# Optimization experiments

Measured on AMD Instinct MI355X. Metric: run time of the kernel, lower is better.

The kernel has to match this reference:

```python
import jax, jax.numpy as jnp
import numpy as np

N, E, B = 50000, 800000, 64
IN_C, HID, HEADS = 128, 64, 4
NEG_SLOPE = 0.2


def _gat_layer(x, src, dst, W, a_src, a_dst, bias, heads, out_c, concat):
    # x: [N, F_in] -> h: [N, heads, out_c]
    h = (x @ W).reshape(-1, heads, out_c)
    alpha_src = jnp.sum(h * a_src[None], axis=-1)  # [N, heads]
    alpha_dst = jnp.sum(h * a_dst[None], axis=-1)  # [N, heads]
    e = jax.nn.leaky_relu(alpha_src[src] + alpha_dst[dst], NEG_SLOPE)  # [Etot, heads]
    # segment softmax over incoming edges of each destination node
    m = jax.lax.stop_gradient(jax.ops.segment_max(e, dst, num_segments=N))
    m = jnp.where(jnp.isfinite(m), m, 0.0)
    ex = jnp.exp(e - m[dst])
    denom = jax.ops.segment_sum(ex, dst, num_segments=N)
    alpha = ex / jnp.maximum(denom[dst], 1e-16)
    msg = h[src] * alpha[:, :, None]  # [Etot, heads, out_c]
    out = jax.ops.segment_sum(msg, dst, num_segments=N)  # [N, heads, out_c]
    if concat:
        return out.reshape(-1, heads * out_c) + bias
    return out.mean(axis=1) + bias


def setup_inputs() -> dict:
    key = jax.random.key(0)
    ks = jax.random.split(key, 16)
    g = lambda k, shp, fan: jax.random.normal(k, shp, jnp.float32) * (1.0 / np.sqrt(fan))
    return {
        "x": jax.random.normal(ks[0], (N, IN_C), jnp.float32),
        "edge_index": jax.random.randint(ks[1], (2, E), 0, N, jnp.int64),
        "batch": jnp.sort(jax.random.randint(ks[2], (N,), 0, B, jnp.int64)),
        "W1": g(ks[3], (IN_C, HEADS * HID), IN_C),
        "as1": g(ks[4], (HEADS, HID), HID),
        "ad1": g(ks[5], (HEADS, HID), HID),
        "b1": jnp.zeros((HEADS * HID,), jnp.float32),
        "W2": g(ks[6], (HEADS * HID, HEADS * HID), HEADS * HID),
        "as2": g(ks[7], (HEADS, HID), HID),
        "ad2": g(ks[8], (HEADS, HID), HID),
        "b2": jnp.zeros((HID,), jnp.float32),
        "Wm1": g(ks[9], (HID, HID), HID),
        "bm1": jnp.zeros((HID,), jnp.float32),
        "Wm2": g(ks[10], (HID, 1), HID),
        "bm2": jnp.zeros((1,), jnp.float32),
    }


def reference(x, edge_index, batch, W1, as1, ad1, b1, W2, as2, ad2, b2, Wm1, bm1, Wm2, bm2):
    # add self loops (PyG GATConv default)
    loops = jnp.arange(N, dtype=edge_index.dtype)
    src = jnp.concatenate([edge_index[0], loops])
    dst = jnp.concatenate([edge_index[1], loops])
    h = _gat_layer(x, src, dst, W1, as1, ad1, b1, HEADS, HID, concat=True)
    h = jax.nn.relu(h)
    h = _gat_layer(h, src, dst, W2, as2, ad2, b2, HEADS, HID, concat=False)
    # global mean pool over graphs
    counts = jax.ops.segment_sum(jnp.ones((N,), h.dtype), batch, num_segments=B)
    pooled = jax.ops.segment_sum(h, batch, num_segments=B) / jnp.maximum(counts, 1.0)[:, None]
    # graph MLP
    out = jax.nn.relu(pooled @ Wm1 + bm1) @ Wm2 + bm2  # [B, 1]
    return out
```

## Files before the change

kernel.cpp:

```cpp
#include <hip/hip_runtime.h>
#include <hip/hip_bf16.h>

#define N_NODES 50000
#define N_EDGES 800000
#define ETOT    (N_EDGES + N_NODES)
#define NB      64
#define IN_C    128
#define HID     64
#define HEADS   4
#define F1      (HEADS * HID)
#define NEG     0.2f
#define SCAN_NBLK ((N_NODES + 255) / 256)

typedef __attribute__((ext_vector_type(8))) short  short8v;
typedef __attribute__((ext_vector_type(4))) float  float4v;

__device__ __forceinline__ float lrelu(float x) { return x >= 0.f ? x : NEG * x; }

__device__ __forceinline__ unsigned short f2bf(float f) {
    unsigned u = __float_as_uint(f);
    u += 0x7FFFu + ((u >> 16) & 1u);
    return (unsigned short)(u >> 16);
}
__device__ __forceinline__ float bf2f(unsigned short h) {
    return __uint_as_float(((unsigned)h) << 16);
}

__global__ void deg_kernel(const int* __restrict__ ei, int* __restrict__ deg) {
    int e = blockIdx.x * 256 + threadIdx.x;
    if (e >= ETOT) return;
    int d = (e < N_EDGES) ? ei[N_EDGES + e] : (e - N_EDGES);
    atomicAdd(&deg[d], 1);
}

__global__ void scan1_kernel(const int* __restrict__ deg, int* __restrict__ part) {
    __shared__ int sh[256];
    int t = threadIdx.x;
    int i = blockIdx.x * 256 + t;
    sh[t] = (i < N_NODES) ? deg[i] : 0;
    __syncthreads();
    #pragma unroll
    for (int o = 128; o; o >>= 1) {
        if (t < o) sh[t] += sh[t + o];
        __syncthreads();
    }
    if (t == 0) part[blockIdx.x] = sh[0];
}

__global__ void scan2_kernel(int* __restrict__ part, int* __restrict__ off) {
    __shared__ int sh[256];
    int t = threadIdx.x;
    int v = (t < SCAN_NBLK) ? part[t] : 0;
    sh[t] = v;
    __syncthreads();
    #pragma unroll
    for (int o = 1; o < 256; o <<= 1) {
        int u = (t >= o) ? sh[t - o] : 0;
        __syncthreads();
        sh[t] += u;
        __syncthreads();
    }
    if (t < SCAN_NBLK) part[t] = sh[t] - v;
    if (t == 255) off[N_NODES] = sh[255];
}

__global__ void scan3_kernel(int* __restrict__ deg, const int* __restrict__ part,
                             int* __restrict__ off) {
    __shared__ int sh[256];
    int t = threadIdx.x;
    int i = blockIdx.x * 256 + t;
    int v = (i < N_NODES) ? deg[i] : 0;
    sh[t] = v;
    __syncthreads();
    #pragma unroll
    for (int o = 1; o < 256; o <<= 1) {
        int u = (t >= o) ? sh[t - o] : 0;
        __syncthreads();
        sh[t] += u;
        __syncthreads();
    }
    if (i < N_NODES) {
        off[i] = part[blockIdx.x] + sh[t] - v;
        deg[i] = 0;
    }
}

__global__ void scatter_kernel(const int* __restrict__ ei, const int* __restrict__ off,
                               int* __restrict__ cursor, int* __restrict__ esrc) {
    int e = blockIdx.x * 256 + threadIdx.x;
    if (e >= ETOT) return;
    int s, d;
    if (e < N_EDGES) { s = ei[e]; d = ei[N_EDGES + e]; }
    else             { s = d = e - N_EDGES; }
    int pos = off[d] + atomicAdd(&cursor[d], 1);
    esrc[pos] = s;
}

__global__ void convw2_kernel(const float* __restrict__ W1,
                              unsigned short* __restrict__ W1h, unsigned short* __restrict__ W1l,
                              const float* __restrict__ W2,
                              unsigned short* __restrict__ W2h, unsigned short* __restrict__ W2l) {
    int i = blockIdx.x * 256 + threadIdx.x;
    const int N1 = IN_C * 256;
    if (i < N1) {
        int k = i >> 8, n = i & 255;
        float v = W1[i];
        unsigned short h = f2bf(v);
        W1h[n * IN_C + k] = h;
        W1l[n * IN_C + k] = f2bf(v - bf2f(h));
    } else {
        int j = i - N1;
        if (j >= F1 * 256) return;
        int k = j >> 8, n = j & 255;
        float v = W2[j];
        unsigned short h = f2bf(v);
        W2h[n * F1 + k] = h;
        W2l[n * F1 + k] = f2bf(v - bf2f(h));
    }
}

template <bool SPLIT_A>
__global__ __launch_bounds__(256) void gemm_mfma(const float* __restrict__ Af32,
                                                 const unsigned short* __restrict__ Abg,
                                                 const unsigned short* __restrict__ Wth,
                                                 const unsigned short* __restrict__ Wtl,
                                                 const float* __restrict__ a_s,
                                                 const float* __restrict__ a_d,
                                                 unsigned short* __restrict__ Cb,
                                                 float* __restrict__ asrcO,
                                                 float* __restrict__ adstO,
                                                 int M, int K) {
    __shared__ unsigned short Ab[64][40];
    __shared__ unsigned short Bh[256][40], Bl[256][40];
    int t  = threadIdx.x;
    int m0 = blockIdx.x * 64;
    int w  = t >> 6, l = t & 63;
    int lr = l & 15, lk = (l >> 4) * 8;

    float asv[4], adv[4];
    #pragma unroll
    for (int nf = 0; nf < 4; ++nf) {
        asv[nf] = a_s[w * 64 + nf * 16 + lr];
        adv[nf] = a_d[w * 64 + nf * 16 + lr];
    }

    float4v acc[4][4];
    #pragma unroll
    for (int mf = 0; mf < 4; ++mf)
        #pragma unroll
        for (int nf = 0; nf < 4; ++nf)
            acc[mf][nf] = (float4v){0.f, 0.f, 0.f, 0.f};

    for (int k0 = 0; k0 < K; k0 += 32) {
        if (SPLIT_A) {
            #pragma unroll
            for (int p = 0; p < 2; ++p) {
                int idx = t + p * 256;
                int r = idx >> 3, c4 = (idx & 7) * 4;
                int gr = m0 + r;
                float4 v = make_float4(0.f, 0.f, 0.f, 0.f);
                if (gr < M) v = *(const float4*)&Af32[(size_t)gr * K + k0 + c4];
                ushort4 hi;
                hi.x = f2bf(v.x); hi.y = f2bf(v.y); hi.z = f2bf(v.z); hi.w = f2bf(v.w);
                *(ushort4*)&Ab[r][c4] = hi;
            }
        } else {
            int r = t >> 2, c8 = (t & 3) * 8;
            int gr = m0 + r;
            short8v vh = {0,0,0,0,0,0,0,0};
            if (gr < M) vh = *(const short8v*)&Abg[(size_t)gr * K + k0 + c8];
            *(short8v*)&Ab[r][c8] = vh;
        }
        #pragma unroll
        for (int p = 0; p < 4; ++p) {
            int idx = t + p * 256;
            int r = idx >> 2, c8 = (idx & 3) * 8;
            short8v vh = *(const short8v*)&Wth[(size_t)r * K + k0 + c8];
            short8v vl = *(const short8v*)&Wtl[(size_t)r * K + k0 + c8];
            *(short8v*)&Bh[r][c8] = vh;
            *(short8v*)&Bl[r][c8] = vl;
        }
        __syncthreads();

        short8v a_f[4], b_hf[4], b_lf[4];
        #pragma unroll
        for (int mf = 0; mf < 4; ++mf)
            a_f[mf] = *(short8v*)&Ab[mf * 16 + lr][lk];
        #pragma unroll
        for (int nf = 0; nf < 4; ++nf) {
            b_hf[nf] = *(short8v*)&Bh[w * 64 + nf * 16 + lr][lk];
            b_lf[nf] = *(short8v*)&Bl[w * 64 + nf * 16 + lr][lk];
        }
        #pragma unroll
        for (int mf = 0; mf < 4; ++mf)
            #pragma unroll
            for (int nf = 0; nf < 4; ++nf) {
                acc[mf][nf] = __builtin_amdgcn_mfma_f32_16x16x32_bf16(a_f[mf], b_hf[nf], acc[mf][nf], 0, 0, 0);
                acc[mf][nf] = __builtin_amdgcn_mfma_f32_16x16x32_bf16(a_f[mf], b_lf[nf], acc[mf][nf], 0, 0, 0);
            }
        __syncthreads();
    }

    #pragma unroll
    for (int mf = 0; mf < 4; ++mf)
        #pragma unroll
        for (int r = 0; r < 4; ++r) {
            float ps = acc[mf][0][r] * asv[0] + acc[mf][1][r] * asv[1]
                     + acc[mf][2][r] * asv[2] + acc[mf][3][r] * asv[3];
            float pd = acc[mf][0][r] * adv[0] + acc[mf][1][r] * adv[1]
                     + acc[mf][2][r] * adv[2] + acc[mf][3][r] * adv[3];
            #pragma unroll
            for (int o = 8; o; o >>= 1) {
                ps += __shfl_xor(ps, o);
                pd += __shfl_xor(pd, o);
            }
            int gr = m0 + mf * 16 + (l >> 4) * 4 + r;
            if (lr == 0 && gr < M) {
                asrcO[gr * 4 + w] = ps;
                adstO[gr * 4 + w] = pd;
            }
        }

    #pragma unroll
    for (int mf = 0; mf < 4; ++mf)
        #pragma unroll
        for (int nf = 0; nf < 4; ++nf)
            #pragma unroll
            for (int r = 0; r < 4; ++r) {
                int gr = m0 + mf * 16 + (l >> 4) * 4 + r;
                if (gr < M) Cb[(size_t)gr * F1 + w * 64 + nf * 16 + lr] = f2bf(acc[mf][nf][r]);
            }
}

template <int LAYER>
__global__ void agg_kernel(const unsigned short* __restrict__ hb,
                           const float* __restrict__ asrc,
                           const float* __restrict__ adst,
                           const int* __restrict__ off,
                           const int* __restrict__ esrc,
                           const float* __restrict__ bias,
                           float* __restrict__ outF,
                           unsigned short* __restrict__ oh) {
    __shared__ int   soff[64];
    __shared__ float cf[64][4];
    int d    = blockIdx.x;
    int lane = threadIdx.x;
    int w    = lane >> 4;
    int e0 = off[d], e1 = off[d + 1];
    float4 ad = *(const float4*)(adst + (size_t)d * 4);
    float den = 0.f;
    float a0 = 0.f, a1 = 0.f, a2 = 0.f, a3 = 0.f;
    const char* hbase = (const char*)hb;
    int lb = lane * 8;

    for (int base = e0; base < e1; base += 64) {
        int cnt = min(64, e1 - base);
        if (lane < cnt) {
            int s = esrc[base + lane];
            soff[lane] = s * (F1 * 2);
            float4 as = *(const float4*)(asrc + (size_t)s * 4);
            cf[lane][0] = __expf(lrelu(as.x + ad.x));
            cf[lane][1] = __expf(lrelu(as.y + ad.y));
            cf[lane][2] = __expf(lrelu(as.z + ad.z));
            cf[lane][3] = __expf(lrelu(as.w + ad.w));
        }
        __syncthreads();
        int i = 0;
        for (; i + 4 <= cnt; i += 4) {
            int o0 = soff[i], o1 = soff[i + 1], o2 = soff[i + 2], o3 = soff[i + 3];
            ushort4 h0 = *(const ushort4*)(hbase + o0 + lb);
            ushort4 h1 = *(const ushort4*)(hbase + o1 + lb);
            ushort4 h2 = *(const ushort4*)(hbase + o2 + lb);
            ushort4 h3 = *(const ushort4*)(hbase + o3 + lb);
            float c0 = cf[i][w], c1 = cf[i + 1][w], c2 = cf[i + 2][w], c3 = cf[i + 3][w];
            den += (c0 + c1) + (c2 + c3);
            a0 += c0 * bf2f(h0.x) + c1 * bf2f(h1.x) + c2 * bf2f(h2.x) + c3 * bf2f(h3.x);
            a1 += c0 * bf2f(h0.y) + c1 * bf2f(h1.y) + c2 * bf2f(h2.y) + c3 * bf2f(h3.y);
            a2 += c0 * bf2f(h0.z) + c1 * bf2f(h1.z) + c2 * bf2f(h2.z) + c3 * bf2f(h3.z);
            a3 += c0 * bf2f(h0.w) + c1 * bf2f(h1.w) + c2 * bf2f(h2.w) + c3 * bf2f(h3.w);
        }
        for (; i < cnt; ++i) {
            int o = soff[i];
            float c = cf[i][w];
            ushort4 hv = *(const ushort4*)(hbase + o + lb);
            den += c;
            a0 += c * bf2f(hv.x);
            a1 += c * bf2f(hv.y);
            a2 += c * bf2f(hv.z);
            a3 += c * bf2f(hv.w);
        }
        __syncthreads();
    }

    float r = 1.f / fmaxf(den, 1e-16f);
    if (LAYER == 1) {
        ushort4 hi;
        hi.x = f2bf(fmaxf(a0 * r + bias[lane * 4 + 0], 0.f));
        hi.y = f2bf(fmaxf(a1 * r + bias[lane * 4 + 1], 0.f));
        hi.z = f2bf(fmaxf(a2 * r + bias[lane * 4 + 2], 0.f));
        hi.w = f2bf(fmaxf(a3 * r + bias[lane * 4 + 3], 0.f));
        *(ushort4*)&oh[(size_t)d * F1 + lane * 4] = hi;
    } else {
        float v0 = a0 * r, v1 = a1 * r, v2 = a2 * r, v3 = a3 * r;
        v0 += __shfl_xor(v0, 16); v0 += __shfl_xor(v0, 32);
        v1 += __shfl_xor(v1, 16); v1 += __shfl_xor(v1, 32);
        v2 += __shfl_xor(v2, 16); v2 += __shfl_xor(v2, 32);
        v3 += __shfl_xor(v3, 16); v3 += __shfl_xor(v3, 32);
        if (lane < 16) {
            float4 o;
            o.x = 0.25f * v0 + bias[lane * 4 + 0];
            o.y = 0.25f * v1 + bias[lane * 4 + 1];
            o.z = 0.25f * v2 + bias[lane * 4 + 2];
            o.w = 0.25f * v3 + bias[lane * 4 + 3];
            *(float4*)&outF[(size_t)d * HID + lane * 4] = o;
        }
    }
}

__device__ __forceinline__ int lowerb(const int* __restrict__ a, int n, int v) {
    int lo = 0, hi = n;
    while (lo < hi) { int m = (lo + hi) >> 1; if (a[m] < v) lo = m + 1; else hi = m; }
    return lo;
}

__global__ void poolmlp_kernel(const float* __restrict__ h2,
                               const int* __restrict__ batch,
                               const float* __restrict__ Wm1, const float* __restrict__ bm1,
                               const float* __restrict__ Wm2, const float* __restrict__ bm2,
                               float* __restrict__ out) {
    __shared__ float sh[4][HID];
    int b = blockIdx.x;
    int t = threadIdx.x, w = t >> 6, c = t & 63;
    int lo = lowerb(batch, N_NODES, b);
    int hi = lowerb(batch, N_NODES, b + 1);
    float s = 0.f;
    for (int n = lo + w; n < hi; n += 4) s += h2[(size_t)n * HID + c];
    sh[w][c] = s;
    __syncthreads();
    if (w == 0) {
        float inv = 1.f / fmaxf((float)(hi - lo), 1.f);
        float P = (sh[0][c] + sh[1][c] + sh[2][c] + sh[3][c]) * inv;
        sh[0][c] = P;
        float s1 = bm1[c];
        #pragma unroll
        for (int k = 0; k < HID; ++k) s1 += sh[0][k] * Wm1[k * HID + c];
        float r = fmaxf(s1, 0.f) * Wm2[c];
        #pragma unroll
        for (int o = 32; o; o >>= 1) r += __shfl_xor(r, o);
        if (c == 0) out[b] = r + bm2[0];
    }
}

extern "C" void kernel_launch(void* const* d_in, const int* in_sizes, int n_in,
                              void* d_out, int out_size, void* d_ws, size_t ws_size,
                              hipStream_t stream) {
    const float* x   = (const float*)d_in[0];
    const int*   ei  = (const int*)d_in[1];
    const int*   bat = (const int*)d_in[2];
    const float* W1  = (const float*)d_in[3];
    const float* as1 = (const float*)d_in[4];
    const float* ad1 = (const float*)d_in[5];
    const float* b1  = (const float*)d_in[6];
    const float* W2  = (const float*)d_in[7];
    const float* as2 = (const float*)d_in[8];
    const float* ad2 = (const float*)d_in[9];
    const float* b2  = (const float*)d_in[10];
    const float* Wm1 = (const float*)d_in[11];
    const float* bm1 = (const float*)d_in[12];
    const float* Wm2 = (const float*)d_in[13];
    const float* bm2 = (const float*)d_in[14];
    float* out = (float*)d_out;

    char* ws = (char*)d_ws;
    size_t cursor = 0;
    auto alloc = [&](size_t bytes) {
        void* p = ws + cursor;
        cursor += (bytes + 511) & ~(size_t)511;
        return p;
    };
    int*   deg    = (int*)alloc((size_t)N_NODES * 4);
    int*   off    = (int*)alloc((size_t)(N_NODES + 1) * 4);
    int*   part   = (int*)alloc((size_t)SCAN_NBLK * 4);
    int*   esrc   = (int*)alloc((size_t)ETOT * 4);
    unsigned short* bufHb = (unsigned short*)alloc((size_t)N_NODES * F1 * 2);
    char*  U      = (char*)alloc((size_t)N_NODES * F1 * 4);
    unsigned short* oh = (unsigned short*)U;
    float* bufO   = (float*)U;
    float* asrc   = (float*)alloc((size_t)N_NODES * HEADS * 4);
    float* adst   = (float*)alloc((size_t)N_NODES * HEADS * 4);
    unsigned short* W1th = (unsigned short*)alloc((size_t)256 * IN_C * 2);
    unsigned short* W1tl = (unsigned short*)alloc((size_t)256 * IN_C * 2);
    unsigned short* W2th = (unsigned short*)alloc((size_t)256 * F1 * 2);
    unsigned short* W2tl = (unsigned short*)alloc((size_t)256 * F1 * 2);

    hipMemsetAsync(deg, 0, (size_t)N_NODES * 4, stream);

    deg_kernel<<<(ETOT + 255) / 256, 256, 0, stream>>>(ei, deg);
    scan1_kernel<<<SCAN_NBLK, 256, 0, stream>>>(deg, part);
    scan2_kernel<<<1, 256, 0, stream>>>(part, off);
    scan3_kernel<<<SCAN_NBLK, 256, 0, stream>>>(deg, part, off);
    scatter_kernel<<<(ETOT + 255) / 256, 256, 0, stream>>>(ei, off, deg, esrc);

    convw2_kernel<<<((IN_C + F1) * 256 + 255) / 256, 256, 0, stream>>>(
        W1, W1th, W1tl, W2, W2th, W2tl);

    const int GB = (N_NODES + 63) / 64;
    gemm_mfma<true><<<GB, 256, 0, stream>>>(x, nullptr, W1th, W1tl,
                                            as1, ad1, bufHb, asrc, adst, N_NODES, IN_C);
    agg_kernel<1><<<N_NODES, 64, 0, stream>>>(bufHb, asrc, adst, off, esrc, b1,
                                              nullptr, oh);

    gemm_mfma<false><<<GB, 256, 0, stream>>>(nullptr, oh, W2th, W2tl,
                                             as2, ad2, bufHb, asrc, adst, N_NODES, F1);
    agg_kernel<2><<<N_NODES, 64, 0, stream>>>(bufHb, asrc, adst, off, esrc, b2,
                                              bufO, nullptr);

    poolmlp_kernel<<<NB, 256, 0, stream>>>(bufO, bat, Wm1, bm1, Wm2, bm2, out);
}
```

Before: 343.3 us.

## Fuse CSR build and weight conversion into one cooperative kernel with grid syncs

Replaces the memset, degree count, three scan kernels, scatter and weight-conversion launches with a single cooperative kernel of 1024 blocks, separating the phases with grid-wide syncs. The aim is to cut the launch and drain overhead of several small dependent kernels. In exchange the work runs at a fixed grid size, each grid.sync adds its own cost, and the launch fails if 1024 blocks cannot be co-resident.

New measurement: 856.2 us. 149% more time.

```diff
diff --git a/kernel.cpp b/kernel.cpp
--- a/kernel.cpp
+++ b/kernel.cpp
@@ -1,5 +1,8 @@
 #include <hip/hip_runtime.h>
 #include <hip/hip_bf16.h>
+#include <hip/hip_cooperative_groups.h>
+
+namespace cg = cooperative_groups;
 
 #define N_NODES 50000
 #define N_EDGES 800000
@@ -11,6 +14,7 @@
 #define F1      (HEADS * HID)
 #define NEG     0.2f
 #define SCAN_NBLK ((N_NODES + 255) / 256)
+#define PREP_BLOCKS 1024
 
 typedef __attribute__((ext_vector_type(8))) short  short8v;
 typedef __attribute__((ext_vector_type(4))) float  float4v;
@@ -26,96 +30,100 @@
     return __uint_as_float(((unsigned)h) << 16);
 }
 
-__global__ void deg_kernel(const int* __restrict__ ei, int* __restrict__ deg) {
-    int e = blockIdx.x * 256 + threadIdx.x;
-    if (e >= ETOT) return;
-    int d = (e < N_EDGES) ? ei[N_EDGES + e] : (e - N_EDGES);
-    atomicAdd(&deg[d], 1);
-}
-
-__global__ void scan1_kernel(const int* __restrict__ deg, int* __restrict__ part) {
+__global__ void prep_kernel(const int* __restrict__ ei,
+                            const float* __restrict__ W1, const float* __restrict__ W2,
+                            int* __restrict__ deg, int* __restrict__ off,
+                            int* __restrict__ part, int* __restrict__ esrc,
+                            unsigned short* __restrict__ W1h, unsigned short* __restrict__ W1l,
+                            unsigned short* __restrict__ W2h, unsigned short* __restrict__ W2l) {
+    cg::grid_group grid = cg::this_grid();
     __shared__ int sh[256];
-    int t = threadIdx.x;
-    int i = blockIdx.x * 256 + t;
-    sh[t] = (i < N_NODES) ? deg[i] : 0;
-    __syncthreads();
-    #pragma unroll
-    for (int o = 128; o; o >>= 1) {
-        if (t < o) sh[t] += sh[t + o];
-        __syncthreads();
-    }
-    if (t == 0) part[blockIdx.x] = sh[0];
-}
-
-__global__ void scan2_kernel(int* __restrict__ part, int* __restrict__ off) {
-    __shared__ int sh[256];
-    int t = threadIdx.x;
-    int v = (t < SCAN_NBLK) ? part[t] : 0;
-    sh[t] = v;
-    __syncthreads();
-    #pragma unroll
-    for (int o = 1; o < 256; o <<= 1) {
-        int u = (t >= o) ? sh[t - o] : 0;
-        __syncthreads();
-        sh[t] += u;
-        __syncthreads();
-    }
-    if (t < SCAN_NBLK) part[t] = sh[t] - v;
-    if (t == 255) off[N_NODES] = sh[255];
-}
-
-__global__ void scan3_kernel(int* __restrict__ deg, const int* __restrict__ part,
-                             int* __restrict__ off) {
-    __shared__ int sh[256];
-    int t = threadIdx.x;
-    int i = blockIdx.x * 256 + t;
-    int v = (i < N_NODES) ? deg[i] : 0;
-    sh[t] = v;
-    __syncthreads();
-    #pragma unroll
-    for (int o = 1; o < 256; o <<= 1) {
-        int u = (t >= o) ? sh[t - o] : 0;
-        __syncthreads();
-        sh[t] += u;
-        __syncthreads();
-    }
-    if (i < N_NODES) {
-        off[i] = part[blockIdx.x] + sh[t] - v;
-        deg[i] = 0;
-    }
-}
-
-__global__ void scatter_kernel(const int* __restrict__ ei, const int* __restrict__ off,
-                               int* __restrict__ cursor, int* __restrict__ esrc) {
-    int e = blockIdx.x * 256 + threadIdx.x;
-    if (e >= ETOT) return;
-    int s, d;
-    if (e < N_EDGES) { s = ei[e]; d = ei[N_EDGES + e]; }
-    else             { s = d = e - N_EDGES; }
-    int pos = off[d] + atomicAdd(&cursor[d], 1);
-    esrc[pos] = s;
-}
-
-__global__ void convw2_kernel(const float* __restrict__ W1,
-                              unsigned short* __restrict__ W1h, unsigned short* __restrict__ W1l,
-                              const float* __restrict__ W2,
-                              unsigned short* __restrict__ W2h, unsigned short* __restrict__ W2l) {
-    int i = blockIdx.x * 256 + threadIdx.x;
-    const int N1 = IN_C * 256;
-    if (i < N1) {
-        int k = i >> 8, n = i & 255;
-        float v = W1[i];
-        unsigned short h = f2bf(v);
-        W1h[n * IN_C + k] = h;
-        W1l[n * IN_C + k] = f2bf(v - bf2f(h));
-    } else {
-        int j = i - N1;
-        if (j >= F1 * 256) return;
-        int k = j >> 8, n = j & 255;
-        float v = W2[j];
-        unsigned short h = f2bf(v);
-        W2h[n * F1 + k] = h;
-        W2l[n * F1 + k] = f2bf(v - bf2f(h));
+    int t   = threadIdx.x;
+    int tid = blockIdx.x * 256 + t;
+    const int NT = PREP_BLOCKS * 256;
+
+    for (int i = tid; i < N_NODES; i += NT) deg[i] = 0;
+    {
+        const int N1 = IN_C * 256;
+        for (int i = tid; i < N1 + F1 * 256; i += NT) {
+            if (i < N1) {
+                int k = i >> 8, n = i & 255;
+                float v = W1[i];
+                unsigned short h = f2bf(v);
+                W1h[n * IN_C + k] = h;
+                W1l[n * IN_C + k] = f2bf(v - bf2f(h));
+            } else {
+                int j = i - N1;
+                int k = j >> 8, n = j & 255;
+                float v = W2[j];
+                unsigned short h = f2bf(v);
+                W2h[n * F1 + k] = h;
+                W2l[n * F1 + k] = f2bf(v - bf2f(h));
+            }
+        }
+    }
+    grid.sync();
+
+    for (int e = tid; e < ETOT; e += NT) {
+        int d = (e < N_EDGES) ? ei[N_EDGES + e] : (e - N_EDGES);
+        atomicAdd(&deg[d], 1);
+    }
+    grid.sync();
+
+    if (blockIdx.x < SCAN_NBLK) {
+        int i = blockIdx.x * 256 + t;
+        sh[t] = (i < N_NODES) ? deg[i] : 0;
+        __syncthreads();
+        #pragma unroll
+        for (int o = 128; o; o >>= 1) {
+            if (t < o) sh[t] += sh[t + o];
+            __syncthreads();
+        }
+        if (t == 0) part[blockIdx.x] = sh[0];
+    }
+    grid.sync();
+
+    if (blockIdx.x == 0) {
+        int v = (t < SCAN_NBLK) ? part[t] : 0;
+        sh[t] = v;
+        __syncthreads();
+        #pragma unroll
+        for (int o = 1; o < 256; o <<= 1) {
+            int u = (t >= o) ? sh[t - o] : 0;
+            __syncthreads();
+            sh[t] += u;
+            __syncthreads();
+        }
+        if (t < SCAN_NBLK) part[t] = sh[t] - v;
+        if (t == 255) off[N_NODES] = sh[255];
+    }
+    grid.sync();
+
+    if (blockIdx.x < SCAN_NBLK) {
+        int i = blockIdx.x * 256 + t;
+        int v = (i < N_NODES) ? deg[i] : 0;
+        sh[t] = v;
+        __syncthreads();
+        #pragma unroll
+        for (int o = 1; o < 256; o <<= 1) {
+            int u = (t >= o) ? sh[t - o] : 0;
+            __syncthreads();
+            sh[t] += u;
+            __syncthreads();
+        }
+        if (i < N_NODES) {
+            off[i] = part[blockIdx.x] + sh[t] - v;
+            deg[i] = 0;
+        }
+    }
+    grid.sync();
+
+    for (int e = tid; e < ETOT; e += NT) {
+        int s, d;
+        if (e < N_EDGES) { s = ei[e]; d = ei[N_EDGES + e]; }
+        else             { s = d = e - N_EDGES; }
+        int pos = off[d] + atomicAdd(&deg[d], 1);
+        esrc[pos] = s;
     }
 }
 
@@ -393,16 +401,13 @@
     unsigned short* W2th = (unsigned short*)alloc((size_t)256 * F1 * 2);
     unsigned short* W2tl = (unsigned short*)alloc((size_t)256 * F1 * 2);
 
-    hipMemsetAsync(deg, 0, (size_t)N_NODES * 4, stream);
-
-    deg_kernel<<<(ETOT + 255) / 256, 256, 0, stream>>>(ei, deg);
-    scan1_kernel<<<SCAN_NBLK, 256, 0, stream>>>(deg, part);
-    scan2_kernel<<<1, 256, 0, stream>>>(part, off);
-    scan3_kernel<<<SCAN_NBLK, 256, 0, stream>>>(deg, part, off);
-    scatter_kernel<<<(ETOT + 255) / 256, 256, 0, stream>>>(ei, off, deg, esrc);
-
-    convw2_kernel<<<((IN_C + F1) * 256 + 255) / 256, 256, 0, stream>>>(
-        W1, W1th, W1tl, W2, W2th, W2tl);
+    {
+        void* args[] = { (void*)&ei, (void*)&W1, (void*)&W2,
+                         (void*)&deg, (void*)&off, (void*)&part, (void*)&esrc,
+                         (void*)&W1th, (void*)&W1tl, (void*)&W2th, (void*)&W2tl };
+        hipLaunchCooperativeKernel((void*)prep_kernel, dim3(PREP_BLOCKS), dim3(256),
+                                   args, 0, stream);
+    }
 
     const int GB = (N_NODES + 63) / 64;
     gemm_mfma<true><<<GB, 256, 0, stream>>>(x, nullptr, W1th, W1tl,
```

## Fold weight conversion into degree kernel and double GEMM row tile to 128

Applied to the files above, without the earlier changes.

The separate weight-split kernel is removed and its work is folded into the first threads of the degree-counting kernel, saving one launch. The MFMA GEMM now processes 128 rows per block instead of 64, so each loaded tile of the hi/lo weight halves is reused across twice as many A rows. This halves global weight traffic per output row but doubles the accumulator registers (8x4 float4 per thread), which may lower occupancy. It also halves the grid to about 391 blocks, which may underfill the GPU.

After: 377.0 us. 9.8% more time.

```diff
diff --git a/kernel.cpp b/kernel.cpp
--- a/kernel.cpp
+++ b/kernel.cpp
@@ -26,8 +26,27 @@
     return __uint_as_float(((unsigned)h) << 16);
 }
 
-__global__ void deg_kernel(const int* __restrict__ ei, int* __restrict__ deg) {
+__global__ void deg_kernel(const int* __restrict__ ei, int* __restrict__ deg,
+                           const float* __restrict__ W1,
+                           unsigned short* __restrict__ W1h, unsigned short* __restrict__ W1l,
+                           const float* __restrict__ W2,
+                           unsigned short* __restrict__ W2h, unsigned short* __restrict__ W2l) {
     int e = blockIdx.x * 256 + threadIdx.x;
+    const int N1 = IN_C * 256;
+    if (e < N1) {
+        int k = e >> 8, n = e & 255;
+        float v = W1[e];
+        unsigned short h = f2bf(v);
+        W1h[n * IN_C + k] = h;
+        W1l[n * IN_C + k] = f2bf(v - bf2f(h));
+    } else if (e < N1 + F1 * 256) {
+        int j = e - N1;
+        int k = j >> 8, n = j & 255;
+        float v = W2[j];
+        unsigned short h = f2bf(v);
+        W2h[n * F1 + k] = h;
+        W2l[n * F1 + k] = f2bf(v - bf2f(h));
+    }
     if (e >= ETOT) return;
     int d = (e < N_EDGES) ? ei[N_EDGES + e] : (e - N_EDGES);
     atomicAdd(&deg[d], 1);
@@ -94,29 +113,6 @@
     else             { s = d = e - N_EDGES; }
     int pos = off[d] + atomicAdd(&cursor[d], 1);
     esrc[pos] = s;
-}
-
-__global__ void convw2_kernel(const float* __restrict__ W1,
-                              unsigned short* __restrict__ W1h, unsigned short* __restrict__ W1l,
-                              const float* __restrict__ W2,
-                              unsigned short* __restrict__ W2h, unsigned short* __restrict__ W2l) {
-    int i = blockIdx.x * 256 + threadIdx.x;
-    const int N1 = IN_C * 256;
-    if (i < N1) {
-        int k = i >> 8, n = i & 255;
-        float v = W1[i];
-        unsigned short h = f2bf(v);
-        W1h[n * IN_C + k] = h;
-        W1l[n * IN_C + k] = f2bf(v - bf2f(h));
-    } else {
-        int j = i - N1;
-        if (j >= F1 * 256) return;
-        int k = j >> 8, n = j & 255;
-        float v = W2[j];
-        unsigned short h = f2bf(v);
-        W2h[n * F1 + k] = h;
-        W2l[n * F1 + k] = f2bf(v - bf2f(h));
-    }
 }
 
 template <bool SPLIT_A>
@@ -130,10 +126,10 @@
                                                  float* __restrict__ asrcO,
                                                  float* __restrict__ adstO,
                                                  int M, int K) {
-    __shared__ unsigned short Ab[64][40];
+    __shared__ unsigned short Ab[128][40];
     __shared__ unsigned short Bh[256][40], Bl[256][40];
     int t  = threadIdx.x;
-    int m0 = blockIdx.x * 64;
+    int m0 = blockIdx.x * 128;
     int w  = t >> 6, l = t & 63;
     int lr = l & 15, lk = (l >> 4) * 8;
 
@@ -144,9 +140,9 @@
         adv[nf] = a_d[w * 64 + nf * 16 + lr];
     }
 
-    float4v acc[4][4];
-    #pragma unroll
-    for (int mf = 0; mf < 4; ++mf)
+    float4v acc[8][4];
+    #pragma unroll
+    for (int mf = 0; mf < 8; ++mf)
         #pragma unroll
         for (int nf = 0; nf < 4; ++nf)
             acc[mf][nf] = (float4v){0.f, 0.f, 0.f, 0.f};
@@ -154,7 +150,7 @@
     for (int k0 = 0; k0 < K; k0 += 32) {
         if (SPLIT_A) {
             #pragma unroll
-            for (int p = 0; p < 2; ++p) {
+            for (int p = 0; p < 4; ++p) {
                 int idx = t + p * 256;
                 int r = idx >> 3, c4 = (idx & 7) * 4;
                 int gr = m0 + r;
@@ -165,11 +161,15 @@
                 *(ushort4*)&Ab[r][c4] = hi;
             }
         } else {
-            int r = t >> 2, c8 = (t & 3) * 8;
-            int gr = m0 + r;
-            short8v vh = {0,0,0,0,0,0,0,0};
-            if (gr < M) vh = *(const short8v*)&Abg[(size_t)gr * K + k0 + c8];
-            *(short8v*)&Ab[r][c8] = vh;
+            #pragma unroll
+            for (int p = 0; p < 2; ++p) {
+                int idx = t + p * 256;
+                int r = idx >> 2, c8 = (idx & 3) * 8;
+                int gr = m0 + r;
+                short8v vh = {0,0,0,0,0,0,0,0};
+                if (gr < M) vh = *(const short8v*)&Abg[(size_t)gr * K + k0 + c8];
+                *(short8v*)&Ab[r][c8] = vh;
+            }
         }
         #pragma unroll
         for (int p = 0; p < 4; ++p) {
@@ -182,27 +182,26 @@
         }
         __syncthreads();
 
-        short8v a_f[4], b_hf[4], b_lf[4];
-        #pragma unroll
-        for (int mf = 0; mf < 4; ++mf)
-            a_f[mf] = *(short8v*)&Ab[mf * 16 + lr][lk];
+        short8v b_hf[4], b_lf[4];
         #pragma unroll
         for (int nf = 0; nf < 4; ++nf) {
             b_hf[nf] = *(short8v*)&Bh[w * 64 + nf * 16 + lr][lk];
             b_lf[nf] = *(short8v*)&Bl[w * 64 + nf * 16 + lr][lk];
         }
         #pragma unroll
-        for (int mf = 0; mf < 4; ++mf)
+        for (int mf = 0; mf < 8; ++mf) {
+            short8v a_f = *(short8v*)&Ab[mf * 16 + lr][lk];
             #pragma unroll
             for (int nf = 0; nf < 4; ++nf) {
-                acc[mf][nf] = __builtin_amdgcn_mfma_f32_16x16x32_bf16(a_f[mf], b_hf[nf], acc[mf][nf], 0, 0, 0);
-                acc[mf][nf] = __builtin_amdgcn_mfma_f32_16x16x32_bf16(a_f[mf], b_lf[nf], acc[mf][nf], 0, 0, 0);
-            }
-        __syncthreads();
-    }
-
-    #pragma unroll
-    for (int mf = 0; mf < 4; ++mf)
+                acc[mf][nf] = __builtin_amdgcn_mfma_f32_16x16x32_bf16(a_f, b_hf[nf], acc[mf][nf], 0, 0, 0);
+                acc[mf][nf] = __builtin_amdgcn_mfma_f32_16x16x32_bf16(a_f, b_lf[nf], acc[mf][nf], 0, 0, 0);
+            }
+        }
+        __syncthreads();
+    }
+
+    #pragma unroll
+    for (int mf = 0; mf < 8; ++mf)
         #pragma unroll
         for (int r = 0; r < 4; ++r) {
             float ps = acc[mf][0][r] * asv[0] + acc[mf][1][r] * asv[1]
@@ -222,7 +221,7 @@
         }
 
     #pragma unroll
-    for (int mf = 0; mf < 4; ++mf)
+    for (int mf = 0; mf < 8; ++mf)
         #pragma unroll
         for (int nf = 0; nf < 4; ++nf)
             #pragma unroll
@@ -395,16 +394,14 @@
 
     hipMemsetAsync(deg, 0, (size_t)N_NODES * 4, stream);
 
-    deg_kernel<<<(ETOT + 255) / 256, 256, 0, stream>>>(ei, deg);
+    deg_kernel<<<(ETOT + 255) / 256, 256, 0, stream>>>(ei, deg, W1, W1th, W1tl,
+                                                       W2, W2th, W2tl);
     scan1_kernel<<<SCAN_NBLK, 256, 0, stream>>>(deg, part);
     scan2_kernel<<<1, 256, 0, stream>>>(part, off);
     scan3_kernel<<<SCAN_NBLK, 256, 0, stream>>>(deg, part, off);
     scatter_kernel<<<(ETOT + 255) / 256, 256, 0, stream>>>(ei, off, deg, esrc);
 
-    convw2_kernel<<<((IN_C + F1) * 256 + 255) / 256, 256, 0, stream>>>(
-        W1, W1th, W1tl, W2, W2th, W2tl);
-
-    const int GB = (N_NODES + 63) / 64;
+    const int GB = (N_NODES + 127) / 128;
     gemm_mfma<true><<<GB, 256, 0, stream>>>(x, nullptr, W1th, W1tl,
                                             as1, ad1, bufHb, asrc, adst, N_NODES, IN_C);
     agg_kernel<1><<<N_NODES, 64, 0, stream>>>(bufHb, asrc, adst, off, esrc, b1,
```
